# Kernel optimization log

Measured on AMD Instinct MI355X. Metric: run time of the kernel, lower is better.

Reference implementation:

```python
import jax, jax.numpy as jnp
import numpy as np

B, S, D, H, L = 16, 1024, 512, 8, 3
NUM_Q, NUM_C, TOTAL_RES = 10000, 300, 2


def setup_inputs() -> dict:
    k = jax.random.split(jax.random.key(0), 20)
    n = lambda i, s, sc=0.02: jax.random.normal(k[i], s, jnp.float32) * sc
    z = lambda: jnp.zeros((D,), jnp.float32)
    o = lambda: jnp.ones((D,), jnp.float32)
    return {
        'in_ex': jax.random.randint(k[0], (B, S), 0, NUM_Q),
        'in_cat': jax.random.randint(k[1], (B, S), 0, NUM_C),
        'in_res': jax.random.randint(k[2], (B, S), 0, 2),
        'in_pos': n(3, (B, S, D)),
        'en_out': n(4, (B, S, D)),
        'E_res': n(5, (TOTAL_RES + 1, D)),
        'E_ex': n(6, (2 * NUM_Q + 1, D)),
        'E_cat': n(7, (2 * NUM_C + 1, D)),
        'g1': o(), 'be1': z(), 'g2': o(), 'be2': z(), 'g3': o(), 'be3': z(),
        'Wq1': n(8, (D, D)), 'bq1': z(), 'Wk1': n(9, (D, D)), 'bk1': z(),
        'Wv1': n(10, (D, D)), 'bv1': z(), 'Wo1': n(11, (D, D)), 'bo1': z(),
        'Wq2': n(12, (D, D)), 'bq2': z(), 'Wk2': n(13, (D, D)), 'bk2': z(),
        'Wv2': n(14, (D, D)), 'bv2': z(), 'Wo2': n(15, (D, D)), 'bo2': z(),
        'fW1': n(16, (D, D)), 'fb1': z(), 'fW2': n(17, (D, D)), 'fb2': z(),
    }


def layer_norm(x, g, b, eps=1e-5):
    m = x.mean(-1, keepdims=True)
    v = ((x - m) ** 2).mean(-1, keepdims=True)
    return (x - m) / jnp.sqrt(v + eps) * g + b


def pyr_attn(q_in, kv_in, Wq, bq, Wk, bk, Wv, bv, Wo, bo):
    # q_in, kv_in: (S, B, D) as in nn.MultiheadAttention convention
    Sq, Bq, Dm = q_in.shape
    dh = Dm // H
    heads = lambda x: x.reshape(x.shape[0], Bq, H, dh).transpose(1, 2, 0, 3)  # (B,H,S,dh)
    qh = heads(q_in @ Wq + bq)
    kh = heads(kv_in @ Wk + bk)
    vh = heads(kv_in @ Wv + bv)
    Skv = kv_in.shape[0]
    i = jnp.arange(Sq)[:, None]
    Ks, Vs, Ms = [], [], []
    for l in range(L):  # pyramid levels: keys/values avg-pooled by 2**l
        f = 2 ** l
        nb = Skv // f
        Ks.append(kh[:, :, :nb * f].reshape(Bq, H, nb, f, dh).mean(3))
        Vs.append(vh[:, :, :nb * f].reshape(Bq, H, nb, f, dh).mean(3))
        # causal: query i may attend pooled block j only if the block ends at or before i
        Ms.append(i >= (jnp.arange(nb)[None, :] + 1) * f - 1)
    K = jnp.concatenate(Ks, 2)
    V = jnp.concatenate(Vs, 2)
    M = jnp.concatenate(Ms, 1)  # (Sq, K_total) multi-level causal mask
    sc = jnp.einsum('bhqd,bhkd->bhqk', qh, K) / np.sqrt(dh).astype(np.float32)
    sc = jnp.where(M[None, None], sc, -1e9)
    a = jax.nn.softmax(sc, -1)
    out = jnp.einsum('bhqk,bhkd->bhqd', a, V)
    return out.transpose(2, 0, 1, 3).reshape(Sq, Bq, Dm) @ Wo + bo


def reference(in_ex, in_cat, in_res, in_pos, en_out, E_res, E_ex, E_cat,
              g1, be1, g2, be2, g3, be3,
              Wq1, bq1, Wk1, bk1, Wv1, bv1, Wo1, bo1,
              Wq2, bq2, Wk2, bk2, Wv2, bv2, Wo2, bo2,
              fW1, fb1, fW2, fb2):
    # embedding sum (first_block=True)
    out = E_res[in_res] + E_ex[in_ex + NUM_Q * in_res] + E_cat[in_cat + NUM_C * in_res] + in_pos
    out = out.transpose(1, 0, 2)  # (S, B, D)
    out = layer_norm(out, g1, be1)
    out = out + pyr_attn(out, out, Wq1, bq1, Wk1, bk1, Wv1, bv1, Wo1, bo1)
    en = layer_norm(en_out.transpose(1, 0, 2), g2, be2)
    out = out + pyr_attn(out, en, Wq2, bq2, Wk2, bk2, Wv2, bv2, Wo2, bo2)
    out = out.transpose(1, 0, 2)  # (B, S, D)
    out = layer_norm(out, g3, be3)
    out = out + (jax.nn.relu(out @ fW1 + fb1) @ fW2 + fb2)
    return out
```

## Files before the change

### kernel.cpp

```cpp
#include <hip/hip_runtime.h>


#define BB 16
#define SS 1024
#define DD 512
#define HH 8
#define DH 64
#define KTOT 1792
#define NROW (BB*SS)
#define KSW 80

typedef unsigned short u16;
typedef __attribute__((ext_vector_type(8))) u16 u16x8;
typedef __attribute__((ext_vector_type(4))) u16 u16x4;
typedef __attribute__((ext_vector_type(8))) short s16x8;
typedef __attribute__((ext_vector_type(4))) float f32x4;

__device__ __forceinline__ float b2f(u16 u) {
    return __uint_as_float(((unsigned int)u) << 16);
}
__device__ __forceinline__ u16 f2b(float f) {
    unsigned int u = __float_as_uint(f);
    return (u16)((u + 0x7FFF + ((u >> 16) & 1)) >> 16);
}
__device__ __forceinline__ s16x8 u2s8(u16x8 u) {
    union { u16x8 u; s16x8 s; } x; x.u = u; return x.s;
}
__device__ __forceinline__ f32x4 mfma16(s16x8 a, s16x8 b, f32x4 c) {
    return __builtin_amdgcn_mfma_f32_16x16x32_bf16(a, b, c, 0, 0, 0);
}
__device__ __forceinline__ float wave_sum(float v) {
    #pragma unroll
    for (int m = 1; m < 64; m <<= 1) v += __shfl_xor(v, m, 64);
    return v;
}
__device__ __forceinline__ float exp2a(float x) {
    float r;
    asm("v_exp_f32 %0, %1" : "=v"(r) : "v"(x));
    return r;
}
__device__ __forceinline__ unsigned int cvtpk(float a, float b) {
    unsigned int r;
    asm("v_cvt_pk_bf16_f32 %0, %1, %2" : "=v"(r) : "v"(a), "v"(b));
    return r;
}
__device__ __forceinline__ void gl16(const void* g, void* l) {
    __builtin_amdgcn_global_load_lds(
        (const __attribute__((address_space(1))) void*)(unsigned long long)g,
        (__attribute__((address_space(3))) void*)(unsigned int)(unsigned long long)l,
        16, 0, 0);
}

__global__ __launch_bounds__(256) void embed_ln_k(
    const int* __restrict__ in_ex, const int* __restrict__ in_cat,
    const int* __restrict__ in_res, const float* __restrict__ in_pos,
    const float* __restrict__ E_res, const float* __restrict__ E_ex,
    const float* __restrict__ E_cat, const float* __restrict__ g,
    const float* __restrict__ be, float* __restrict__ out)
{
    int wave = threadIdx.x >> 6, lane = threadIdx.x & 63;
    int row = blockIdx.x * 4 + wave;
    int res = in_res[row];
    int ex  = in_ex[row] + 10000 * res;
    int cat = in_cat[row] + 300 * res;
    int d0 = lane * 8;
    const float* pr = &E_res[(size_t)res * DD + d0];
    const float* pe = &E_ex[(size_t)ex * DD + d0];
    const float* pc = &E_cat[(size_t)cat * DD + d0];
    const float* pp = &in_pos[(size_t)row * DD + d0];
    float x[8]; float s = 0.f;
    #pragma unroll
    for (int j = 0; j < 8; j++) { x[j] = pr[j] + pe[j] + pc[j] + pp[j]; s += x[j]; }
    s = wave_sum(s);
    float mean = s * (1.0f / DD);
    float vs = 0.f;
    #pragma unroll
    for (int j = 0; j < 8; j++) { float d = x[j] - mean; vs += d * d; }
    vs = wave_sum(vs);
    float rstd = rsqrtf(vs * (1.0f / DD) + 1e-5f);
    #pragma unroll
    for (int j = 0; j < 8; j++)
        out[(size_t)row * DD + d0 + j] = (x[j] - mean) * rstd * g[d0 + j] + be[d0 + j];
}

template<bool OUTB>
__global__ __launch_bounds__(256) void ln_k(
    const float* __restrict__ x, const float* __restrict__ g,
    const float* __restrict__ be, void* __restrict__ outv)
{
    int wave = threadIdx.x >> 6, lane = threadIdx.x & 63;
    int row = blockIdx.x * 4 + wave;
    int d0 = lane * 8;
    const float* px = &x[(size_t)row * DD + d0];
    float xv[8]; float s = 0.f;
    #pragma unroll
    for (int j = 0; j < 8; j++) { xv[j] = px[j]; s += xv[j]; }
    s = wave_sum(s);
    float mean = s * (1.0f / DD);
    float vs = 0.f;
    #pragma unroll
    for (int j = 0; j < 8; j++) { float d = xv[j] - mean; vs += d * d; }
    vs = wave_sum(vs);
    float rstd = rsqrtf(vs * (1.0f / DD) + 1e-5f);
    #pragma unroll
    for (int j = 0; j < 8; j++) {
        float v = (xv[j] - mean) * rstd * g[d0 + j] + be[d0 + j];
        if (OUTB) ((u16*)outv)[(size_t)row * DD + d0 + j] = f2b(v);
        else      ((float*)outv)[(size_t)row * DD + d0 + j] = v;
    }
}

__global__ __launch_bounds__(256) void transpose_k(const float* __restrict__ src, u16* __restrict__ dst)
{
    int idx = blockIdx.x * 256 + threadIdx.x;
    int n = idx & 511, k = idx >> 9;
    dst[n * 512 + k] = f2b(src[k * 512 + n]);
}

__global__ __launch_bounds__(256) void pool_k12_k(u16* __restrict__ KP)
{
    int idx = blockIdx.x * 256 + threadIdx.x;
    int d = idx & 63;
    int t = idx >> 6;
    int k12 = t % 768;
    int bh = t / 768;
    int s0, f;
    if (k12 < 512) { s0 = 2 * k12; f = 2; } else { s0 = 4 * (k12 - 512); f = 4; }
    size_t base = (size_t)bh * KTOT * DH;
    float acc = 0.f;
    for (int i = 0; i < f; i++)
        acc += b2f(KP[base + (size_t)(s0 + i) * DH + d]);
    KP[base + (size_t)(1024 + k12) * DH + d] = f2b(acc * (1.0f / (float)f));
}

__global__ __launch_bounds__(256) void pool_vt_k(const u16* __restrict__ Vp, u16* __restrict__ VPt)
{
    __shared__ __align__(16) u16 T[64 * 72];
    int tid = threadIdx.x;
    int st = blockIdx.x;
    int h  = blockIdx.y;
    int b  = blockIdx.z;
    int s0 = st * 64;
    {
        const u16* src = &Vp[((size_t)(b * SS + s0)) * DD + h * DH];
        #pragma unroll
        for (int it = 0; it < 2; it++) {
            int idx = it * 256 + tid;
            int row = idx >> 3, unit = idx & 7;
            *(u16x8*)&T[row * 72 + unit * 8] =
                *(const u16x8*)&src[(size_t)row * DD + unit * 8];
        }
    }
    __syncthreads();
    int d = tid & 63, g = tid >> 6;
    size_t obase = ((size_t)(b * HH + h) * DH + d) * KTOT;
    #pragma unroll
    for (int gg = 0; gg < 2; gg++) {
        int grp = g * 2 + gg;
        u16x8 v;
        #pragma unroll
        for (int j = 0; j < 8; j++) v[j] = T[(grp * 8 + j) * 72 + d];
        *(u16x8*)&VPt[obase + s0 + grp * 8] = v;
    }
    {
        u16x8 v;
        #pragma unroll
        for (int j = 0; j < 8; j++) {
            int sl = g * 8 + j;
            float a = b2f(T[(2 * sl) * 72 + d]) + b2f(T[(2 * sl + 1) * 72 + d]);
            v[j] = f2b(a * 0.5f);
        }
        *(u16x8*)&VPt[obase + 1024 + st * 32 + g * 8] = v;
    }
    {
        u16x4 v;
        #pragma unroll
        for (int j = 0; j < 4; j++) {
            int s2 = g * 4 + j;
            float a = 0.f;
            #pragma unroll
            for (int i = 0; i < 4; i++) a += b2f(T[(4 * s2 + i) * 72 + d]);
            v[j] = f2b(a * 0.25f);
        }
        *(u16x4*)&VPt[obase + 1536 + st * 16 + g * 4] = v;
    }
}

template<bool AF32, bool RELU, bool RES, bool OUTB, bool KLAY>
__global__ __launch_bounds__(256) void gemm_k(
    const void* __restrict__ Av, const u16* __restrict__ Wt,
    const float* __restrict__ bias, const float* __restrict__ resid,
    void* __restrict__ Cv, int M, int K, float oscale)
{
    const int N = 512;
    constexpr int ASW = AF32 ? 40 : 32;
    __shared__ __align__(16) u16 As[2][128 * ASW];
    __shared__ __align__(16) u16 Bs[2][128 * 32];
    int tid = threadIdx.x;
    int wave = tid >> 6, lane = tid & 63;
    int quad = lane >> 4, l16 = lane & 15;
    int m0 = blockIdx.y * 128, n0 = blockIdx.x * 128;
    int wm = (wave >> 1) * 64, wn = (wave & 1) * 64;
    int r = tid >> 1, cg = (tid & 1) * 16;
    int grow = wave * 16 + (lane >> 2);
    int gk = (lane & 3) * 8;
    const float* Af = (const float*)Av;
    const u16*  Ab = (const u16*)Av;
    f32x4 acc[4][4];
    #pragma unroll
    for (int i = 0; i < 4; i++)
        #pragma unroll
        for (int j = 0; j < 4; j++)
            #pragma unroll
            for (int rr = 0; rr < 4; rr++) acc[i][j][rr] = 0.f;

    const int NT = K >> 5;
    f32x4 s0, s1, s2, s3;

    #define ISSUE_B(t, buf) { int k0_ = (t) << 5; \
        gl16(&Wt[(size_t)(n0 + grow) * 512 + k0_ + gk],      &Bs[buf][grow * 32 + gk]); \
        gl16(&Wt[(size_t)(n0 + 64 + grow) * 512 + k0_ + gk], &Bs[buf][(64 + grow) * 32 + gk]); }
    #define ISSUE_A16(t, buf) { int k0_ = (t) << 5; \
        gl16(&Ab[(size_t)(m0 + grow) * K + k0_ + gk],      &As[buf][grow * 32 + gk]); \
        gl16(&Ab[(size_t)(m0 + 64 + grow) * K + k0_ + gk], &As[buf][(64 + grow) * 32 + gk]); }
    #define LOAD_A32(t) { const float* src_ = &Af[(size_t)(m0 + r) * K + ((t) << 5) + cg]; \
        s0 = *(const f32x4*)&src_[0];  s1 = *(const f32x4*)&src_[4]; \
        s2 = *(const f32x4*)&src_[8];  s3 = *(const f32x4*)&src_[12]; }
    #define WRITE_A32(buf) { union { unsigned int w[4]; u16x8 v; } L_, H_; \
        L_.w[0] = cvtpk(s0[0], s0[1]); L_.w[1] = cvtpk(s0[2], s0[3]); \
        L_.w[2] = cvtpk(s1[0], s1[1]); L_.w[3] = cvtpk(s1[2], s1[3]); \
        H_.w[0] = cvtpk(s2[0], s2[1]); H_.w[1] = cvtpk(s2[2], s2[3]); \
        H_.w[2] = cvtpk(s3[0], s3[1]); H_.w[3] = cvtpk(s3[2], s3[3]); \
        *(u16x8*)&As[buf][r * ASW + cg]     = L_.v; \
        *(u16x8*)&As[buf][r * ASW + cg + 8] = H_.v; }

    if (AF32) { LOAD_A32(0); WRITE_A32(0); }
    else      { ISSUE_A16(0, 0); }
    ISSUE_B(0, 0);
    __syncthreads();

    for (int t = 0; t < NT; ++t) {
        int cur = t & 1, nxt = cur ^ 1;
        if (t + 1 < NT) {
            if (AF32) { LOAD_A32(t + 1); }
            else      { ISSUE_A16(t + 1, nxt); }
            ISSUE_B(t + 1, nxt);
        }
        s16x8 af[4], bfr[4];
        #pragma unroll
        for (int i = 0; i < 4; i++)
            af[i] = u2s8(*(const u16x8*)&As[cur][(wm + i * 16 + l16) * ASW + quad * 8]);
        #pragma unroll
        for (int j = 0; j < 4; j++)
            bfr[j] = u2s8(*(const u16x8*)&Bs[cur][(wn + j * 16 + l16) * 32 + quad * 8]);
        #pragma unroll
        for (int i = 0; i < 4; i++)
            #pragma unroll
            for (int j = 0; j < 4; j++)
                acc[i][j] = mfma16(af[i], bfr[j], acc[i][j]);
        if (AF32 && t + 1 < NT) { WRITE_A32(nxt); }
        __syncthreads();
    }
    #undef ISSUE_B
    #undef ISSUE_A16
    #undef LOAD_A32
    #undef WRITE_A32

    #pragma unroll
    for (int j = 0; j < 4; j++) {
        int col = n0 + wn + j * 16 + l16;
        float bv = bias[col];
        #pragma unroll
        for (int i = 0; i < 4; i++) {
            int rowb = m0 + wm + i * 16 + quad * 4;
            #pragma unroll
            for (int rr = 0; rr < 4; rr++) {
                float v = (acc[i][j][rr] + bv) * oscale;
                if (RELU) v = fmaxf(v, 0.f);
                int row = rowb + rr;
                if (RES) v += resid[(size_t)row * N + col];
                if (KLAY) {
                    int b_ = row >> 10, s_ = row & 1023;
                    size_t dst = (((size_t)(b_ * HH + (col >> 6)) * KTOT) + s_) * DH + (col & 63);
                    ((u16*)Cv)[dst] = f2b(v);
                } else if (OUTB) {
                    ((u16*)Cv)[(size_t)row * N + col] = f2b(v);
                } else {
                    ((float*)Cv)[(size_t)row * N + col] = v;
                }
            }
        }
    }
}

__global__ __launch_bounds__(512) void attn_k(
    const u16* __restrict__ Qp, const u16* __restrict__ KP,
    const u16* __restrict__ VPt, u16* __restrict__ Hout)
{
    __shared__ __align__(16) u16 Ksh[64 * KSW];
    __shared__ __align__(16) u16 Vsh[64 * KSW];
    int tid = threadIdx.x;
    int wave = tid >> 6, lane = tid & 63;
    int quad = lane >> 4, l16 = lane & 15;
    int id = blockIdx.x;
    int h = id & 7;
    int inner = id >> 3;
    int x = inner & 3, b = inner >> 2;

    int t0 = x + 4 * wave;
    int tiles[2] = { t0, 63 - t0 };

    const u16* Kb = KP  + ((size_t)(b * HH + h)) * KTOT * DH;
    const u16* Vt = VPt + ((size_t)(b * HH + h)) * DH * KTOT;

    s16x8 qa[2][2];
    f32x4 o[2][4];
    float lrun[2] = {0.f, 0.f};
    #pragma unroll
    for (int c = 0; c < 2; c++) {
        int q0 = tiles[c] * 16;
        const u16* qrow = Qp + ((size_t)(b * SS + q0 + l16)) * DD + h * DH;
        qa[c][0] = u2s8(*(const u16x8*)&qrow[quad * 8]);
        qa[c][1] = u2s8(*(const u16x8*)&qrow[32 + quad * 8]);
        #pragma unroll
        for (int j = 0; j < 4; j++)
            #pragma unroll
            for (int r = 0; r < 4; r++) o[c][j][r] = 0.f;
    }

    int row0 = 8 * (l16 >> 2) + (l16 & 3);

    int srow = tid >> 3, sunit = tid & 7;
    u16x8 kreg = *(const u16x8*)&Kb[(size_t)tid * 8];
    u16x8 vreg = *(const u16x8*)&Vt[(size_t)srow * KTOT + sunit * 8];

    for (int ch = 0; ch < 28; ch++) {
        int kbase = ch * 64;
        int lv = (ch < 16) ? 0 : (ch < 24) ? 1 : 2;
        __syncthreads();
        *(u16x8*)&Ksh[srow * KSW + sunit * 8] = kreg;
        *(u16x8*)&Vsh[srow * KSW + sunit * 8] = vreg;
        __syncthreads();
        if (ch + 1 < 28) {
            int nb = (ch + 1) * 64;
            kreg = *(const u16x8*)&Kb[(size_t)nb * DH + tid * 8];
            vreg = *(const u16x8*)&Vt[(size_t)srow * KTOT + nb + sunit * 8];
        }

        #pragma unroll
        for (int c = 0; c < 2; c++) {
            int q0 = tiles[c] * 16;
            int qmax = q0 + 15;
            int efirst = (lv == 0) ? kbase
                       : (lv == 1) ? 2 * (kbase - 1024) + 1
                                   : 4 * (kbase - 1536) + 3;
            if (efirst > qmax) continue;

            int elast = (lv == 0) ? kbase + 63
                      : (lv == 1) ? 2 * (kbase + 63 - 1024) + 1
                                  : 4 * (kbase + 63 - 1536) + 3;

            f32x4 zt[4];
            __builtin_amdgcn_s_setprio(1);
            #pragma unroll
            for (int t = 0; t < 4; t++) {
                const int toff = (t & 1) * 4 + (t >> 1) * 32;
                const u16* kr = &Ksh[(row0 + toff) * KSW];
                s16x8 kf0 = u2s8(*(const u16x8*)&kr[quad * 8]);
                s16x8 kf1 = u2s8(*(const u16x8*)&kr[32 + quad * 8]);
                f32x4 z;
                #pragma unroll
                for (int rr = 0; rr < 4; rr++) z[rr] = 0.f;
                z = mfma16(kf0, qa[c][0], z);
                zt[t] = mfma16(kf1, qa[c][1], z);
            }
            __builtin_amdgcn_s_setprio(0);

            if (elast > q0) {
                int q = q0 + l16;
                int kmaxv = (lv == 0) ? q - kbase
                          : (lv == 1) ? ((q - 1) >> 1) - (kbase - 1024)
                                      : ((q - 3) >> 2) - (kbase - 1536);
                int thrb = kmaxv - 8 * quad;
                #pragma unroll
                for (int t = 0; t < 4; t++) {
                    int thr = thrb - ((t & 1) * 4 + (t >> 1) * 32);
                    #pragma unroll
                    for (int rr = 0; rr < 4; rr++)
                        if (rr > thr) zt[t][rr] = -1e30f;
                }
            }

            float p[4][4]; float ps0 = 0.f, ps1 = 0.f;
            #pragma unroll
            for (int t = 0; t < 4; t++)
                #pragma unroll
                for (int rr = 0; rr < 4; rr++) {
                    p[t][rr] = exp2a(zt[t][rr]);
                    if (t & 1) ps1 += p[t][rr]; else ps0 += p[t][rr];
                }
            float ps = ps0 + ps1;
            ps += __shfl_xor(ps, 16, 64);
            ps += __shfl_xor(ps, 32, 64);
            lrun[c] += ps;

            union { unsigned int w[4]; u16x8 v; } U0, U1;
            U0.w[0] = cvtpk(p[0][0], p[0][1]); U0.w[1] = cvtpk(p[0][2], p[0][3]);
            U0.w[2] = cvtpk(p[1][0], p[1][1]); U0.w[3] = cvtpk(p[1][2], p[1][3]);
            U1.w[0] = cvtpk(p[2][0], p[2][1]); U1.w[1] = cvtpk(p[2][2], p[2][3]);
            U1.w[2] = cvtpk(p[3][0], p[3][1]); U1.w[3] = cvtpk(p[3][2], p[3][3]);
            s16x8 pf0 = u2s8(U0.v), pf1 = u2s8(U1.v);

            __builtin_amdgcn_s_setprio(1);
            #pragma unroll
            for (int j = 0; j < 4; j++) {
                const u16* vr = &Vsh[(j * 16 + l16) * KSW];
                o[c][j] = mfma16(pf0, u2s8(*(const u16x8*)&vr[quad * 8]), o[c][j]);
                o[c][j] = mfma16(pf1, u2s8(*(const u16x8*)&vr[32 + quad * 8]), o[c][j]);
            }
            __builtin_amdgcn_s_setprio(0);
        }
    }

    #pragma unroll
    for (int c = 0; c < 2; c++) {
        int q0 = tiles[c] * 16;
        float il = 1.0f / lrun[c];
        float ilr[4];
        #pragma unroll
        for (int rr = 0; rr < 4; rr++) ilr[rr] = __shfl(il, quad * 4 + rr, 64);
        #pragma unroll
        for (int rr = 0; rr < 4; rr++) {
            int q = q0 + quad * 4 + rr;
            #pragma unroll
            for (int j = 0; j < 4; j++)
                Hout[((size_t)(b * SS + q)) * DD + h * DH + j * 16 + l16] = f2b(o[c][j][rr] * ilr[rr]);
        }
    }
}

extern "C" void kernel_launch(void* const* d_in, const int* in_sizes, int n_in,
                              void* d_out, int out_size, void* d_ws, size_t ws_size,
                              hipStream_t stream)
{
    (void)in_sizes; (void)n_in; (void)out_size; (void)ws_size;
    const int* in_ex  = (const int*)d_in[0];
    const int* in_cat = (const int*)d_in[1];
    const int* in_res = (const int*)d_in[2];
    const float* in_pos = (const float*)d_in[3];
    const float* en_out = (const float*)d_in[4];
    const float* E_res  = (const float*)d_in[5];
    const float* E_ex   = (const float*)d_in[6];
    const float* E_cat  = (const float*)d_in[7];
    const float* g1 = (const float*)d_in[8],  *be1 = (const float*)d_in[9];
    const float* g2 = (const float*)d_in[10], *be2 = (const float*)d_in[11];
    const float* g3 = (const float*)d_in[12], *be3 = (const float*)d_in[13];
    const float* Wq1 = (const float*)d_in[14], *bq1 = (const float*)d_in[15];
    const float* Wk1 = (const float*)d_in[16], *bk1 = (const float*)d_in[17];
    const float* Wv1 = (const float*)d_in[18], *bv1 = (const float*)d_in[19];
    const float* Wo1 = (const float*)d_in[20], *bo1 = (const float*)d_in[21];
    const float* Wq2 = (const float*)d_in[22], *bq2 = (const float*)d_in[23];
    const float* Wk2 = (const float*)d_in[24], *bk2 = (const float*)d_in[25];
    const float* Wv2 = (const float*)d_in[26], *bv2 = (const float*)d_in[27];
    const float* Wo2 = (const float*)d_in[28], *bo2 = (const float*)d_in[29];
    const float* fW1 = (const float*)d_in[30], *fb1 = (const float*)d_in[31];
    const float* fW2 = (const float*)d_in[32], *fb2 = (const float*)d_in[33];

    char* ws = (char*)d_ws;
    const size_t U = (size_t)NROW * DD * 2;
    float* x1 = (float*)(ws);
    u16* qb   = (u16*)(ws + 2 * U);
    u16* vb   = (u16*)(ws + 3 * U);
    u16* hb   = (u16*)(ws + 4 * U);
    u16* kp   = (u16*)(ws + 5 * U);
    u16* vpt  = (u16*)(ws + 5 * U + 7 * U / 4);
    u16* wt   = (u16*)(ws + 8 * U + U / 2);
    float* x2 = (float*)d_out;
    u16* en = (u16*)(ws);
    float* x3 = x1;
    float* x4 = (float*)(ws + 5 * U);
    u16* ff1 = hb;

    const float* wsrc[10] = {Wq1, Wk1, Wv1, Wo1, Wq2, Wk2, Wv2, Wo2, fW1, fW2};
    for (int i = 0; i < 10; i++)
        transpose_k<<<1024, 256, 0, stream>>>(wsrc[i], wt + (size_t)i * 262144);
    u16* tWq1 = wt,            *tWk1 = wt + 262144,   *tWv1 = wt + 2*262144, *tWo1 = wt + 3*262144;
    u16* tWq2 = wt + 4*262144, *tWk2 = wt + 5*262144, *tWv2 = wt + 6*262144, *tWo2 = wt + 7*262144;
    u16* tF1  = wt + 8*262144, *tF2  = wt + 9*262144;

    dim3 ggrid(4, 128);
    dim3 vtgrid(16, 8, 16);
    const float QSC = 0.18033688f;

    embed_ln_k<<<4096, 256, 0, stream>>>(in_ex, in_cat, in_res, in_pos,
                                         E_res, E_ex, E_cat, g1, be1, x1);

    gemm_k<true,false,false,true,false><<<ggrid, 256, 0, stream>>>(x1, tWq1, bq1, nullptr, qb, NROW, 512, QSC);
    gemm_k<true,false,false,true,true ><<<ggrid, 256, 0, stream>>>(x1, tWk1, bk1, nullptr, kp, NROW, 512, 1.0f);
    gemm_k<true,false,false,true,false><<<ggrid, 256, 0, stream>>>(x1, tWv1, bv1, nullptr, vb, NROW, 512, 1.0f);
    pool_k12_k<<<24576, 256, 0, stream>>>(kp);
    pool_vt_k<<<vtgrid, 256, 0, stream>>>(vb, vpt);
    attn_k<<<512, 512, 0, stream>>>(qb, kp, vpt, hb);
    gemm_k<false,false,true,false,false><<<ggrid, 256, 0, stream>>>(hb, tWo1, bo1, x1, x2, NROW, 512, 1.0f);

    ln_k<true><<<4096, 256, 0, stream>>>(en_out, g2, be2, en);
    gemm_k<true,false,false,true,false><<<ggrid, 256, 0, stream>>>(x2, tWq2, bq2, nullptr, qb, NROW, 512, QSC);
    gemm_k<false,false,false,true,true ><<<ggrid, 256, 0, stream>>>(en, tWk2, bk2, nullptr, kp, NROW, 512, 1.0f);
    gemm_k<false,false,false,true,false><<<ggrid, 256, 0, stream>>>(en, tWv2, bv2, nullptr, vb, NROW, 512, 1.0f);
    pool_k12_k<<<24576, 256, 0, stream>>>(kp);
    pool_vt_k<<<vtgrid, 256, 0, stream>>>(vb, vpt);
    attn_k<<<512, 512, 0, stream>>>(qb, kp, vpt, hb);
    gemm_k<false,false,true,false,false><<<ggrid, 256, 0, stream>>>(hb, tWo2, bo2, x2, x3, NROW, 512, 1.0f);

    ln_k<false><<<4096, 256, 0, stream>>>(x3, g3, be3, x4);
    gemm_k<true,true,false,true,false><<<ggrid, 256, 0, stream>>>(x4, tF1, fb1, nullptr, ff1, NROW, 512, 1.0f);
    gemm_k<false,false,true,false,false><<<ggrid, 256, 0, stream>>>(ff1, tF2, fb2, x4, (float*)d_out, NROW, 512, 1.0f);
}
```

Before: 644.1 us.

## Restructure attention to four query tiles per wave with double-buffered K/V LDS

The attention kernel now runs with 256 threads (4 waves) instead of 512, and each wave handles four 16-row query tiles instead of two. K and V fragments are loaded from LDS once per chunk and reused across all four tiles. K/V chunks are double-buffered in shared memory, which leaves a single barrier per chunk and overlaps the global prefetch with compute. In exchange, register pressure rises (four sets of accumulators and P fragments), and there are fewer waves per block to hide latency.

```diff
diff --git a/kernel.cpp b/kernel.cpp
--- a/kernel.cpp
+++ b/kernel.cpp
@@ -293,12 +293,12 @@
     }
 }
 
-__global__ __launch_bounds__(512) void attn_k(
+__global__ __launch_bounds__(256, 2) void attn_k(
     const u16* __restrict__ Qp, const u16* __restrict__ KP,
     const u16* __restrict__ VPt, u16* __restrict__ Hout)
 {
-    __shared__ __align__(16) u16 Ksh[64 * KSW];
-    __shared__ __align__(16) u16 Vsh[64 * KSW];
+    __shared__ __align__(16) u16 Ksh[2][64 * KSW];
+    __shared__ __align__(16) u16 Vsh[2][64 * KSW];
     int tid = threadIdx.x;
     int wave = tid >> 6, lane = tid & 63;
     int quad = lane >> 4, l16 = lane & 15;
@@ -307,131 +307,168 @@
     int inner = id >> 3;
     int x = inner & 3, b = inner >> 2;
 
-    int t0 = x + 4 * wave;
-    int tiles[2] = { t0, 63 - t0 };
+    int wx = x * 4 + wave;
+    int tiles[4] = { wx, 31 - wx, 32 + wx, 63 - wx };
 
     const u16* Kb = KP  + ((size_t)(b * HH + h)) * KTOT * DH;
     const u16* Vt = VPt + ((size_t)(b * HH + h)) * DH * KTOT;
 
-    s16x8 qa[2][2];
-    f32x4 o[2][4];
-    float lrun[2] = {0.f, 0.f};
-    #pragma unroll
-    for (int c = 0; c < 2; c++) {
+    s16x8 qa[4][2];
+    f32x4 o[4][4];
+    float lrun[4];
+    int q0a[4];
+    #pragma unroll
+    for (int c = 0; c < 4; c++) {
         int q0 = tiles[c] * 16;
+        q0a[c] = q0;
+        lrun[c] = 0.f;
         const u16* qrow = Qp + ((size_t)(b * SS + q0 + l16)) * DD + h * DH;
         qa[c][0] = u2s8(*(const u16x8*)&qrow[quad * 8]);
         qa[c][1] = u2s8(*(const u16x8*)&qrow[32 + quad * 8]);
         #pragma unroll
         for (int j = 0; j < 4; j++)
             #pragma unroll
-            for (int r = 0; r < 4; r++) o[c][j][r] = 0.f;
+            for (int rr = 0; rr < 4; rr++) o[c][j][rr] = 0.f;
     }
 
     int row0 = 8 * (l16 >> 2) + (l16 & 3);
 
-    int srow = tid >> 3, sunit = tid & 7;
-    u16x8 kreg = *(const u16x8*)&Kb[(size_t)tid * 8];
-    u16x8 vreg = *(const u16x8*)&Vt[(size_t)srow * KTOT + sunit * 8];
+    int u0 = tid, u1 = 256 + tid;
+    int kr0 = u0 >> 3, ku0 = (u0 & 7) * 8;
+    int kr1 = u1 >> 3, ku1 = (u1 & 7) * 8;
+
+    u16x8 kreg0 = *(const u16x8*)&Kb[(size_t)u0 * 8];
+    u16x8 kreg1 = *(const u16x8*)&Kb[(size_t)u1 * 8];
+    u16x8 vreg0 = *(const u16x8*)&Vt[(size_t)kr0 * KTOT + ku0];
+    u16x8 vreg1 = *(const u16x8*)&Vt[(size_t)kr1 * KTOT + ku1];
+    *(u16x8*)&Ksh[0][kr0 * KSW + ku0] = kreg0;
+    *(u16x8*)&Ksh[0][kr1 * KSW + ku1] = kreg1;
+    *(u16x8*)&Vsh[0][kr0 * KSW + ku0] = vreg0;
+    *(u16x8*)&Vsh[0][kr1 * KSW + ku1] = vreg1;
+    __syncthreads();
 
     for (int ch = 0; ch < 28; ch++) {
+        int cur = ch & 1;
         int kbase = ch * 64;
         int lv = (ch < 16) ? 0 : (ch < 24) ? 1 : 2;
-        __syncthreads();
-        *(u16x8*)&Ksh[srow * KSW + sunit * 8] = kreg;
-        *(u16x8*)&Vsh[srow * KSW + sunit * 8] = vreg;
-        __syncthreads();
         if (ch + 1 < 28) {
             int nb = (ch + 1) * 64;
-            kreg = *(const u16x8*)&Kb[(size_t)nb * DH + tid * 8];
-            vreg = *(const u16x8*)&Vt[(size_t)srow * KTOT + nb + sunit * 8];
-        }
-
-        #pragma unroll
-        for (int c = 0; c < 2; c++) {
-            int q0 = tiles[c] * 16;
-            int qmax = q0 + 15;
-            int efirst = (lv == 0) ? kbase
-                       : (lv == 1) ? 2 * (kbase - 1024) + 1
-                                   : 4 * (kbase - 1536) + 3;
-            if (efirst > qmax) continue;
-
-            int elast = (lv == 0) ? kbase + 63
-                      : (lv == 1) ? 2 * (kbase + 63 - 1024) + 1
-                                  : 4 * (kbase + 63 - 1536) + 3;
-
-            f32x4 zt[4];
-            __builtin_amdgcn_s_setprio(1);
+            kreg0 = *(const u16x8*)&Kb[(size_t)nb * DH + u0 * 8];
+            kreg1 = *(const u16x8*)&Kb[(size_t)nb * DH + u1 * 8];
+            vreg0 = *(const u16x8*)&Vt[(size_t)kr0 * KTOT + nb + ku0];
+            vreg1 = *(const u16x8*)&Vt[(size_t)kr1 * KTOT + nb + ku1];
+        }
+
+        int efirst = (lv == 0) ? kbase
+                   : (lv == 1) ? 2 * (kbase - 1024) + 1
+                               : 4 * (kbase - 1536) + 3;
+        int elast  = (lv == 0) ? kbase + 63
+                   : (lv == 1) ? 2 * (kbase + 63 - 1024) + 1
+                               : 4 * (kbase + 63 - 1536) + 3;
+        bool act[4];
+        #pragma unroll
+        for (int c = 0; c < 4; c++) act[c] = (efirst <= q0a[c] + 15);
+
+        if (act[0] | act[1] | act[2] | act[3]) {
+            s16x8 fA[4], fB[4];
             #pragma unroll
             for (int t = 0; t < 4; t++) {
                 const int toff = (t & 1) * 4 + (t >> 1) * 32;
-                const u16* kr = &Ksh[(row0 + toff) * KSW];
-                s16x8 kf0 = u2s8(*(const u16x8*)&kr[quad * 8]);
-                s16x8 kf1 = u2s8(*(const u16x8*)&kr[32 + quad * 8]);
-                f32x4 z;
+                const u16* kr = &Ksh[cur][(row0 + toff) * KSW];
+                fA[t] = u2s8(*(const u16x8*)&kr[quad * 8]);
+                fB[t] = u2s8(*(const u16x8*)&kr[32 + quad * 8]);
+            }
+            s16x8 pfa[4], pfb[4];
+            #pragma unroll
+            for (int c = 0; c < 4; c++) {
+                if (!act[c]) continue;
+                f32x4 zt[4];
+                __builtin_amdgcn_s_setprio(1);
                 #pragma unroll
-                for (int rr = 0; rr < 4; rr++) z[rr] = 0.f;
-                z = mfma16(kf0, qa[c][0], z);
-                zt[t] = mfma16(kf1, qa[c][1], z);
+                for (int t = 0; t < 4; t++) {
+                    f32x4 z;
+                    #pragma unroll
+                    for (int rr = 0; rr < 4; rr++) z[rr] = 0.f;
+                    z = mfma16(fA[t], qa[c][0], z);
+                    zt[t] = mfma16(fB[t], qa[c][1], z);
+                }
+                __builtin_amdgcn_s_setprio(0);
+
+                if (elast > q0a[c]) {
+                    int q = q0a[c] + l16;
+                    int kmaxv = (lv == 0) ? q - kbase
+                              : (lv == 1) ? ((q - 1) >> 1) - (kbase - 1024)
+                                          : ((q - 3) >> 2) - (kbase - 1536);
+                    int thrb = kmaxv - 8 * quad;
+                    #pragma unroll
+                    for (int t = 0; t < 4; t++) {
+                        int thr = thrb - ((t & 1) * 4 + (t >> 1) * 32);
+                        #pragma unroll
+                        for (int rr = 0; rr < 4; rr++)
+                            if (rr > thr) zt[t][rr] = -1e30f;
+                    }
+                }
+
+                float p[4][4]; float ps0 = 0.f, ps1 = 0.f;
+                #pragma unroll
+                for (int t = 0; t < 4; t++)
+                    #pragma unroll
+                    for (int rr = 0; rr < 4; rr++) {
+                        p[t][rr] = exp2a(zt[t][rr]);
+                        if (t & 1) ps1 += p[t][rr]; else ps0 += p[t][rr];
+                    }
+                float ps = ps0 + ps1;
+                ps += __shfl_xor(ps, 16, 64);
+                ps += __shfl_xor(ps, 32, 64);
+                lrun[c] += ps;
+
+                union { unsigned int w[4]; u16x8 v; } U0, U1;
+                U0.w[0] = cvtpk(p[0][0], p[0][1]); U0.w[1] = cvtpk(p[0][2], p[0][3]);
+                U0.w[2] = cvtpk(p[1][0], p[1][1]); U0.w[3] = cvtpk(p[1][2], p[1][3]);
+                U1.w[0] = cvtpk(p[2][0], p[2][1]); U1.w[1] = cvtpk(p[2][2], p[2][3]);
+                U1.w[2] = cvtpk(p[3][0], p[3][1]); U1.w[3] = cvtpk(p[3][2], p[3][3]);
+                pfa[c] = u2s8(U0.v); pfb[c] = u2s8(U1.v);
+            }
+
+            s16x8 vA[4], vB[4];
+            #pragma unroll
+            for (int j = 0; j < 4; j++) {
+                const u16* vr = &Vsh[cur][(j * 16 + l16) * KSW];
+                vA[j] = u2s8(*(const u16x8*)&vr[quad * 8]);
+                vB[j] = u2s8(*(const u16x8*)&vr[32 + quad * 8]);
+            }
+            __builtin_amdgcn_s_setprio(1);
+            #pragma unroll
+            for (int c = 0; c < 4; c++) {
+                if (!act[c]) continue;
+                #pragma unroll
+                for (int j = 0; j < 4; j++) {
+                    o[c][j] = mfma16(pfa[c], vA[j], o[c][j]);
+                    o[c][j] = mfma16(pfb[c], vB[j], o[c][j]);
+                }
             }
             __builtin_amdgcn_s_setprio(0);
-
-            if (elast > q0) {
-                int q = q0 + l16;
-                int kmaxv = (lv == 0) ? q - kbase
-                          : (lv == 1) ? ((q - 1) >> 1) - (kbase - 1024)
-                                      : ((q - 3) >> 2) - (kbase - 1536);
-                int thrb = kmaxv - 8 * quad;
-                #pragma unroll
-                for (int t = 0; t < 4; t++) {
-                    int thr = thrb - ((t & 1) * 4 + (t >> 1) * 32);
-                    #pragma unroll
-                    for (int rr = 0; rr < 4; rr++)
-                        if (rr > thr) zt[t][rr] = -1e30f;
-                }
-            }
-
-            float p[4][4]; float ps0 = 0.f, ps1 = 0.f;
-            #pragma unroll
-            for (int t = 0; t < 4; t++)
-                #pragma unroll
-                for (int rr = 0; rr < 4; rr++) {
-                    p[t][rr] = exp2a(zt[t][rr]);
-                    if (t & 1) ps1 += p[t][rr]; else ps0 += p[t][rr];
-                }
-            float ps = ps0 + ps1;
-            ps += __shfl_xor(ps, 16, 64);
-            ps += __shfl_xor(ps, 32, 64);
-            lrun[c] += ps;
-
-            union { unsigned int w[4]; u16x8 v; } U0, U1;
-            U0.w[0] = cvtpk(p[0][0], p[0][1]); U0.w[1] = cvtpk(p[0][2], p[0][3]);
-            U0.w[2] = cvtpk(p[1][0], p[1][1]); U0.w[3] = cvtpk(p[1][2], p[1][3]);
-            U1.w[0] = cvtpk(p[2][0], p[2][1]); U1.w[1] = cvtpk(p[2][2], p[2][3]);
-            U1.w[2] = cvtpk(p[3][0], p[3][1]); U1.w[3] = cvtpk(p[3][2], p[3][3]);
-            s16x8 pf0 = u2s8(U0.v), pf1 = u2s8(U1.v);
-
-            __builtin_amdgcn_s_setprio(1);
-            #pragma unroll
-            for (int j = 0; j < 4; j++) {
-                const u16* vr = &Vsh[(j * 16 + l16) * KSW];
-                o[c][j] = mfma16(pf0, u2s8(*(const u16x8*)&vr[quad * 8]), o[c][j]);
-                o[c][j] = mfma16(pf1, u2s8(*(const u16x8*)&vr[32 + quad * 8]), o[c][j]);
-            }
-            __builtin_amdgcn_s_setprio(0);
-        }
-    }
-
-    #pragma unroll
-    for (int c = 0; c < 2; c++) {
-        int q0 = tiles[c] * 16;
+        }
+
+        if (ch + 1 < 28) {
+            int nxt = cur ^ 1;
+            *(u16x8*)&Ksh[nxt][kr0 * KSW + ku0] = kreg0;
+            *(u16x8*)&Ksh[nxt][kr1 * KSW + ku1] = kreg1;
+            *(u16x8*)&Vsh[nxt][kr0 * KSW + ku0] = vreg0;
+            *(u16x8*)&Vsh[nxt][kr1 * KSW + ku1] = vreg1;
+        }
+        __syncthreads();
+    }
+
+    #pragma unroll
+    for (int c = 0; c < 4; c++) {
         float il = 1.0f / lrun[c];
         float ilr[4];
         #pragma unroll
         for (int rr = 0; rr < 4; rr++) ilr[rr] = __shfl(il, quad * 4 + rr, 64);
         #pragma unroll
         for (int rr = 0; rr < 4; rr++) {
-            int q = q0 + quad * 4 + rr;
+            int q = q0a[c] + quad * 4 + rr;
             #pragma unroll
             for (int j = 0; j < 4; j++)
                 Hout[((size_t)(b * SS + q)) * DD + h * DH + j * 16 + l16] = f2b(o[c][j][rr] * ilr[rr]);
@@ -500,7 +537,7 @@
     gemm_k<true,false,false,true,false><<<ggrid, 256, 0, stream>>>(x1, tWv1, bv1, nullptr, vb, NROW, 512, 1.0f);
     pool_k12_k<<<24576, 256, 0, stream>>>(kp);
     pool_vt_k<<<vtgrid, 256, 0, stream>>>(vb, vpt);
-    attn_k<<<512, 512, 0, stream>>>(qb, kp, vpt, hb);
+    attn_k<<<512, 256, 0, stream>>>(qb, kp, vpt, hb);
     gemm_k<false,false,true,false,false><<<ggrid, 256, 0, stream>>>(hb, tWo1, bo1, x1, x2, NROW, 512, 1.0f);
 
     ln_k<true><<<4096, 256, 0, stream>>>(en_out, g2, be2, en);
@@ -509,7 +546,7 @@
     gemm_k<false,false,false,true,false><<<ggrid, 256, 0, stream>>>(en, tWv2, bv2, nullptr, vb, NROW, 512, 1.0f);
     pool_k12_k<<<24576, 256, 0, stream>>>(kp);
     pool_vt_k<<<vtgrid, 256, 0, stream>>>(vb, vpt);
-    attn_k<<<512, 512, 0, stream>>>(qb, kp, vpt, hb);
+    attn_k<<<512, 256, 0, stream>>>(qb, kp, vpt, hb);
     gemm_k<false,false,true,false,false><<<ggrid, 256, 0, stream>>>(hb, tWo2, bo2, x2, x3, NROW, 512, 1.0f);
 
     ln_k<false><<<4096, 256, 0, stream>>>(x3, g3, be3, x4);
```

Result: no change. 642.3 us (-0.3%).
